# Optimization experiments

Hardware: AMD Instinct MI355X
Metric: run time of the kernel (lower is better)

## Reference

```python
import jax, jax.numpy as jnp
import numpy as np

N_NODES = 50000
N_EDGES = 800000
IN_C, HID_C, OUT_C = 256, 512, 256
DROP_P = 0.5


def _glorot(key, fan_in, fan_out):
    lim = float(np.sqrt(6.0 / (fan_in + fan_out)))
    return jax.random.uniform(key, (fan_in, fan_out), jnp.float32, -lim, lim)


def setup_inputs() -> dict:
    key = jax.random.key(0)
    k_x, k_e, k_w1, k_w2 = jax.random.split(key, 4)
    tensor = jax.random.normal(k_x, (N_NODES, IN_C), dtype=jnp.float32)
    edge_index = jax.random.randint(k_e, (2, N_EDGES), 0, N_NODES, dtype=jnp.int64)
    W1 = _glorot(k_w1, IN_C, HID_C)
    b1 = jnp.zeros((HID_C,), jnp.float32)
    W2 = _glorot(k_w2, HID_C, OUT_C)
    b2 = jnp.zeros((OUT_C,), jnp.float32)
    return {"tensor": tensor, "edge_index": edge_index,
            "W1": W1, "b1": b1, "W2": W2, "b2": b2}


def _gcn_conv(x, W, b, row, col, n_nodes):
    # PyG GCNConv: x' = D^-1/2 (A + I) D^-1/2 (x W) + b
    x = x @ W                                            # [N, F_out]
    # degree over targets including self-loops
    deg = jax.ops.segment_sum(jnp.ones_like(col, dtype=x.dtype), col,
                              num_segments=n_nodes) + 1.0
    dinv = jnp.where(deg > 0, jax.lax.rsqrt(deg), 0.0)   # [N]
    norm = dinv[row] * dinv[col]                         # [E]
    msg = x[row] * norm[:, None]                         # [E, F_out] gather
    out = jax.ops.segment_sum(msg, col, num_segments=n_nodes)  # scatter-add
    out = out + x * (dinv * dinv)[:, None]               # self-loop term
    return out + b


def _dropout(x, key, p=DROP_P):
    keep = jax.random.bernoulli(key, 1.0 - p, x.shape)
    return jnp.where(keep, x / (1.0 - p), 0.0)


def reference(tensor, edge_index, W1, b1, W2, b2):
    row, col = edge_index[0], edge_index[1]
    k1, k2 = jax.random.split(jax.random.key(42))
    x = _gcn_conv(tensor, W1, b1, row, col, N_NODES)
    x = _dropout(jax.nn.relu(x), k1)
    x = _gcn_conv(x, W2, b2, row, col, N_NODES)
    x = _dropout(jax.nn.relu(x), k2)
    return x
```

## Files before the change

### kernel.cpp

```cpp
#include <hip/hip_runtime.h>
#include <stdint.h>


#define N_NODES 50000
#define N_EDGES 800000
#define M_PAD   50048
#define IN_C 256
#define HID_C 512
#define OUT_C 256

typedef __attribute__((ext_vector_type(8))) short bf16x8;
typedef __attribute__((ext_vector_type(4))) float f32x4;

struct U2 { unsigned a, b; };

__host__ __device__ constexpr unsigned rotl32(unsigned x, int d) {
  return (x << d) | (x >> (32 - d));
}

#define TF_ROUND(r) { x0 += x1; x1 = rotl32(x1, (r)); x1 ^= x0; }

__host__ __device__ constexpr U2 threefry2x32(unsigned k0, unsigned k1,
                                              unsigned x0, unsigned x1) {
  unsigned ks2 = k0 ^ k1 ^ 0x1BD11BDAu;
  x0 += k0; x1 += k1;
  TF_ROUND(13) TF_ROUND(15) TF_ROUND(26) TF_ROUND(6)  x0 += k1;  x1 += ks2 + 1u;
  TF_ROUND(17) TF_ROUND(29) TF_ROUND(16) TF_ROUND(24) x0 += ks2; x1 += k0 + 2u;
  TF_ROUND(13) TF_ROUND(15) TF_ROUND(26) TF_ROUND(6)  x0 += k0;  x1 += k1 + 3u;
  TF_ROUND(17) TF_ROUND(29) TF_ROUND(16) TF_ROUND(24) x0 += k1;  x1 += ks2 + 4u;
  TF_ROUND(13) TF_ROUND(15) TF_ROUND(26) TF_ROUND(6)  x0 += ks2; x1 += k0 + 5u;
  return U2{x0, x1};
}

__device__ __forceinline__ ushort f2b(float f) {
  unsigned u = __builtin_bit_cast(unsigned, f);
  unsigned r = (u + 0x7fffu + ((u >> 16) & 1u)) >> 16;
  return (ushort)r;
}
__device__ __forceinline__ float b2f(ushort h) {
  unsigned u = (unsigned)h << 16;
  return __builtin_bit_cast(float, u);
}

__device__ __forceinline__ void gload16(const void* g, void* l) {
  __builtin_amdgcn_global_load_lds(
      (const __attribute__((address_space(1))) void*)g,
      (__attribute__((address_space(3))) void*)l, 16, 0, 0);
}

__global__ void deg_kernel(const int* __restrict__ col, int* __restrict__ cnt, int E) {
  int e = blockIdx.x * 256 + threadIdx.x;
  if (e < E) atomicAdd(&cnt[col[e]], 1);
}

__global__ void dinv_kernel(const int* __restrict__ cnt, float* __restrict__ dinv, int N) {
  int n = blockIdx.x * 256 + threadIdx.x;
  if (n < N) dinv[n] = rsqrtf((float)cnt[n] + 1.0f);
}

__global__ __launch_bounds__(1024) void scan_local(const int* __restrict__ cnt,
                                                   int* __restrict__ indptr,
                                                   int* __restrict__ chunkSums, int n) {
  __shared__ int s[1024];
  int gid = blockIdx.x * 1024 + threadIdx.x;
  int v = (gid < n) ? cnt[gid] : 0;
  s[threadIdx.x] = v;
  __syncthreads();
#pragma unroll
  for (int off = 1; off < 1024; off <<= 1) {
    int t = (threadIdx.x >= off) ? s[threadIdx.x - off] : 0;
    __syncthreads();
    s[threadIdx.x] += t;
    __syncthreads();
  }
  if (gid < n) indptr[gid] = s[threadIdx.x] - v;
  if (threadIdx.x == 1023) chunkSums[blockIdx.x] = s[1023];
}

__global__ void scan_chunks(int* __restrict__ chunkSums, int nChunks) {
  if (threadIdx.x == 0 && blockIdx.x == 0) {
    int acc = 0;
    for (int i = 0; i < nChunks; ++i) { int t = chunkSums[i]; chunkSums[i] = acc; acc += t; }
  }
}

__global__ void add_offsets(int* __restrict__ indptr, const int* __restrict__ chunkSums,
                            int n, int total) {
  int gid = blockIdx.x * 256 + threadIdx.x;
  if (gid < n) indptr[gid] += chunkSums[gid >> 10];
  if (gid == 0) indptr[n] = total;
}

__global__ void build_csr(const int* __restrict__ row, const int* __restrict__ col,
                          const int* __restrict__ indptr, int* __restrict__ cursor,
                          const float* __restrict__ dinv,
                          int2* __restrict__ srcW, int E) {
  int e = blockIdx.x * 256 + threadIdx.x;
  if (e < E) {
    int r = row[e];
    int c = col[e];
    int p = indptr[c] + atomicAdd(&cursor[c], 1);
    srcW[p] = make_int2(r, __builtin_bit_cast(int, dinv[r]));
  }
}

__global__ void cvt_f32_bf16(const float* __restrict__ in, ushort* __restrict__ out, int n4) {
  int i = blockIdx.x * 256 + threadIdx.x;
  if (i < n4) {
    float4 v = *(const float4*)(in + (size_t)i * 4);
    ushort4 o = make_ushort4(f2b(v.x), f2b(v.y), f2b(v.z), f2b(v.w));
    *(ushort4*)(out + (size_t)i * 4) = o;
  }
}

template <int LOGK>
__global__ void wT_kernel(const float* __restrict__ W, ushort* __restrict__ WT, int N, int total) {
  int i = blockIdx.x * 256 + threadIdx.x;
  if (i < total) {
    int k = i & ((1 << LOGK) - 1);
    int n = i >> LOGK;
    WT[i] = f2b(W[(size_t)k * N + n]);
  }
}

#define ROW_ACC(vv, ww)                                                        \
  { a0 += b2f((vv).x) * (ww); a1 += b2f((vv).y) * (ww);                        \
    a2 += b2f((vv).z) * (ww); a3 += b2f((vv).w) * (ww); }

template <bool EPI>
__global__ __launch_bounds__(256) void gather8(const ushort* __restrict__ X,
                                               const int* __restrict__ indptr,
                                               const int2* __restrict__ srcW,
                                               const float* __restrict__ dinv,
                                               const float* __restrict__ bias,
                                               void* __restrict__ outp,
                                               unsigned char* __restrict__ maskGen,
                                               const unsigned char* __restrict__ maskUse,
                                               unsigned kk0, unsigned kk1, int N) {
  int wid = (blockIdx.x * 256 + threadIdx.x) >> 6;
  int lane = threadIdx.x & 63;
  if (wid >= N) return;
  int beg = __builtin_amdgcn_readfirstlane(indptr[wid]);
  int end = __builtin_amdgcn_readfirstlane(indptr[wid + 1]);
  float dc = dinv[wid];
  const int f0 = lane * 4;
  ushort4 sv = *(const ushort4*)(X + (size_t)wid * 256 + f0);
  float a0 = b2f(sv.x) * dc, a1 = b2f(sv.y) * dc,
        a2 = b2f(sv.z) * dc, a3 = b2f(sv.w) * dc;

  int e = beg;
  for (; e + 8 <= end; e += 8) {
    int2 p0 = srcW[e + 0], p1 = srcW[e + 1], p2 = srcW[e + 2], p3 = srcW[e + 3];
    int2 p4 = srcW[e + 4], p5 = srcW[e + 5], p6 = srcW[e + 6], p7 = srcW[e + 7];
    ushort4 v0 = *(const ushort4*)(X + (size_t)p0.x * 256 + f0);
    ushort4 v1 = *(const ushort4*)(X + (size_t)p1.x * 256 + f0);
    ushort4 v2 = *(const ushort4*)(X + (size_t)p2.x * 256 + f0);
    ushort4 v3 = *(const ushort4*)(X + (size_t)p3.x * 256 + f0);
    ushort4 v4 = *(const ushort4*)(X + (size_t)p4.x * 256 + f0);
    ushort4 v5 = *(const ushort4*)(X + (size_t)p5.x * 256 + f0);
    ushort4 v6 = *(const ushort4*)(X + (size_t)p6.x * 256 + f0);
    ushort4 v7 = *(const ushort4*)(X + (size_t)p7.x * 256 + f0);
    ROW_ACC(v0, __builtin_bit_cast(float, p0.y));
    ROW_ACC(v1, __builtin_bit_cast(float, p1.y));
    ROW_ACC(v2, __builtin_bit_cast(float, p2.y));
    ROW_ACC(v3, __builtin_bit_cast(float, p3.y));
    ROW_ACC(v4, __builtin_bit_cast(float, p4.y));
    ROW_ACC(v5, __builtin_bit_cast(float, p5.y));
    ROW_ACC(v6, __builtin_bit_cast(float, p6.y));
    ROW_ACC(v7, __builtin_bit_cast(float, p7.y));
  }
  for (; e + 2 <= end; e += 2) {
    int2 p0 = srcW[e + 0], p1 = srcW[e + 1];
    ushort4 v0 = *(const ushort4*)(X + (size_t)p0.x * 256 + f0);
    ushort4 v1 = *(const ushort4*)(X + (size_t)p1.x * 256 + f0);
    ROW_ACC(v0, __builtin_bit_cast(float, p0.y));
    ROW_ACC(v1, __builtin_bit_cast(float, p1.y));
  }
  if (e < end) {
    int2 p0 = srcW[e];
    ushort4 v0 = *(const ushort4*)(X + (size_t)p0.x * 256 + f0);
    ROW_ACC(v0, __builtin_bit_cast(float, p0.y));
  }
  a0 *= dc; a1 *= dc; a2 *= dc; a3 *= dc;

  if (EPI) {
    float4 bv = *(const float4*)(bias + f0);
    unsigned mk = maskUse[(size_t)wid * 32 + (lane >> 1)];
    int sh = (lane & 1) * 4;
    float v0 = fmaxf(a0 + bv.x, 0.f);
    float v1 = fmaxf(a1 + bv.y, 0.f);
    float v2 = fmaxf(a2 + bv.z, 0.f);
    float v3 = fmaxf(a3 + bv.w, 0.f);
    v0 = ((mk >> (sh + 0)) & 1u) ? 0.f : v0 * 2.0f;
    v1 = ((mk >> (sh + 1)) & 1u) ? 0.f : v1 * 2.0f;
    v2 = ((mk >> (sh + 2)) & 1u) ? 0.f : v2 * 2.0f;
    v3 = ((mk >> (sh + 3)) & 1u) ? 0.f : v3 * 2.0f;
    *(float4*)((float*)outp + (size_t)wid * 256 + f0) = make_float4(v0, v1, v2, v3);
  } else {
    uint2 o;
    o.x = (unsigned)f2b(a0) | ((unsigned)f2b(a1) << 16);
    o.y = (unsigned)f2b(a2) | ((unsigned)f2b(a3) << 16);
    *(uint2*)((ushort*)outp + (size_t)wid * 256 + f0) = o;
    unsigned gl = (unsigned)wid * 64u + (unsigned)lane;
    unsigned eb = gl * 8u;
    unsigned byte = 0;
#pragma unroll
    for (int j = 0; j < 8; ++j) {
      U2 r = threefry2x32(kk0, kk1, 0u, eb + (unsigned)j);
      byte |= (((r.a ^ r.b) >> 31) & 1u) << j;
    }
    maskGen[gl] = (unsigned char)byte;
  }
}

template <int MODE>
__global__ __launch_bounds__(256) void gemm_bf16(const ushort* __restrict__ A,
                                                 const ushort* __restrict__ BT,
                                                 ushort* __restrict__ C,
                                                 int M, int K, int N,
                                                 const float* __restrict__ bias,
                                                 const unsigned char* __restrict__ mask1,
                                                 unsigned char* __restrict__ maskOut,
                                                 unsigned kk0, unsigned kk1) {
  __shared__ __align__(16) ushort lds[16384];
  const int tid = threadIdx.x;
  const int lane = tid & 63;
  const int wv = tid >> 6;
  const int wr = wv >> 1, wc = wv & 1;
  const int bm = blockIdx.x * 128;
  const int bn = blockIdx.y * 128;

  f32x4 acc[4][4] = {};
  const int xorv = (lane & 7) << 4;

  const int nt = K >> 6;
  for (int t = 0; t < nt; ++t) {
    const int k0 = t << 6;
#pragma unroll
    for (int l = 0; l < 4; ++l) {
      int cid = l * 256 + tid;
      int row = cid >> 3;
      int kcol = ((cid & 7) ^ (row & 7)) * 8;
      gload16(A + (size_t)(bm + row) * K + k0 + kcol, (void*)(lds + cid * 8));
      gload16(BT + (size_t)(bn + row) * K + k0 + kcol, (void*)(lds + 8192 + cid * 8));
    }
    __syncthreads();
    const char* Ab = (const char*)lds;
    const char* Bb = (const char*)(lds + 8192);
#pragma unroll
    for (int ks = 0; ks < 2; ++ks) {
      bf16x8 af[4], bf[4];
      const int kb = (ks * 64 + (lane >> 4) * 16) ^ xorv;
#pragma unroll
      for (int i = 0; i < 4; ++i) {
        int arow = wr * 64 + i * 16 + (lane & 15);
        af[i] = *(const bf16x8*)(Ab + arow * 128 + kb);
        int brow = wc * 64 + i * 16 + (lane & 15);
        bf[i] = *(const bf16x8*)(Bb + brow * 128 + kb);
      }
#pragma unroll
      for (int m = 0; m < 4; ++m)
#pragma unroll
        for (int n = 0; n < 4; ++n)
          acc[m][n] = __builtin_amdgcn_mfma_f32_16x16x32_bf16(bf[n], af[m], acc[m][n], 0, 0, 0);
    }
    __syncthreads();
  }

  const int growb = bm + wr * 64 + (lane & 15);
  const int gcolb = bn + wc * 64 + ((lane >> 4) << 2);
  float4 bias_v[4];
  if (MODE == 1) {
#pragma unroll
    for (int n = 0; n < 4; ++n) bias_v[n] = *(const float4*)(bias + gcolb + n * 16);
  }
#pragma unroll
  for (int m = 0; m < 4; ++m) {
    int grow = growb + m * 16;
    unsigned long long mrow = 0;
    if (MODE == 1)
      mrow = *(const unsigned long long*)(mask1 + (((size_t)grow * N + bn + wc * 64) >> 3));
#pragma unroll
    for (int n = 0; n < 4; ++n) {
      int gcol = gcolb + n * 16;
      float v[4];
#pragma unroll
      for (int r = 0; r < 4; ++r) {
        float x = acc[m][n][r];
        if (MODE == 1) {
          x = fmaxf(x + ((const float*)&bias_v[n])[r], 0.f);
          int bit = (gcol - (bn + wc * 64)) + r;
          x = ((mrow >> bit) & 1ull) ? 0.f : x * 2.0f;
        }
        v[r] = x;
      }
      uint2 o;
      o.x = (unsigned)f2b(v[0]) | ((unsigned)f2b(v[1]) << 16);
      o.y = (unsigned)f2b(v[2]) | ((unsigned)f2b(v[3]) << 16);
      *(uint2*)(C + (size_t)grow * N + gcol) = o;
    }
  }

  if (MODE == 2) {
    int row = tid >> 1, ch = (tid & 1) * 64;
    int grow = bm + row;
    unsigned base = (unsigned)grow * (unsigned)N + (unsigned)(bn + ch);
    unsigned long long mword = 0;
#pragma unroll
    for (int j = 0; j < 64; ++j) {
      U2 rr = threefry2x32(kk0, kk1, 0u, base + (unsigned)j);
      mword |= (unsigned long long)(((rr.a ^ rr.b) >> 31) & 1u) << j;
    }
    *(unsigned long long*)(maskOut + (size_t)(base >> 3)) = mword;
  }
}

extern "C" void kernel_launch(void* const* d_in, const int* in_sizes, int n_in,
                              void* d_out, int out_size, void* d_ws, size_t ws_size,
                              hipStream_t stream) {
  const float* x  = (const float*)d_in[0];
  const int*   ei = (const int*)d_in[1];
  const float* W1 = (const float*)d_in[2];
  const float* b1 = (const float*)d_in[3];
  const float* W2 = (const float*)d_in[4];
  const float* b2 = (const float*)d_in[5];
  float* out = (float*)d_out;
  (void)in_sizes; (void)n_in; (void)out_size; (void)ws_size;

  const int* row = ei;
  const int* col = ei + N_EDGES;

  char* ws = (char*)d_ws;
  float*  dinv      = (float*) (ws);
  int*    cnt       = (int*)   (ws + (1u << 18));
  int*    indptr    = (int*)   (ws + (2u << 18));
  int*    cursor    = (int*)   (ws + (3u << 18));
  int*    chunkSums = (int*)   (ws + (1u << 20));
  int2*   srcW      = (int2*)  (ws + 2u * (1u << 20));
  ushort* W1T       = (ushort*)(ws + 9u * (1u << 20));
  ushort* W2T       = (ushort*)(ws + 9u * (1u << 20) + (1u << 19));
  unsigned char* mask1 = (unsigned char*)(ws + 10u * (1u << 20));
  unsigned char* mask2 = (unsigned char*)(ws + 14u * (1u << 20));
  ushort* x16       = (ushort*)(ws + 18u * (1u << 20));
  ushort* aggB      = (ushort*)(ws + 44u * (1u << 20));
  ushort* h         = (ushort*)(ws + 70u * (1u << 20));
  ushort* hw2       = (ushort*)(ws + 122u* (1u << 20));

  constexpr U2 K1 = threefry2x32(0u, 42u, 0u, 0u);
  constexpr U2 K2 = threefry2x32(0u, 42u, 0u, 1u);

  (void)hipMemsetAsync(cnt, 0, N_NODES * sizeof(int), stream);
  (void)hipMemsetAsync(cursor, 0, N_NODES * sizeof(int), stream);
  deg_kernel<<<(N_EDGES + 255) / 256, 256, 0, stream>>>(col, cnt, N_EDGES);
  dinv_kernel<<<(N_NODES + 255) / 256, 256, 0, stream>>>(cnt, dinv, N_NODES);
  const int nChunks = (N_NODES + 1023) / 1024;
  scan_local<<<nChunks, 1024, 0, stream>>>(cnt, indptr, chunkSums, N_NODES);
  scan_chunks<<<1, 64, 0, stream>>>(chunkSums, nChunks);
  add_offsets<<<(N_NODES + 255) / 256, 256, 0, stream>>>(indptr, chunkSums, N_NODES, N_EDGES);
  build_csr<<<(N_EDGES + 255) / 256, 256, 0, stream>>>(row, col, indptr, cursor, dinv, srcW, N_EDGES);

  cvt_f32_bf16<<<(N_NODES * IN_C / 4 + 255) / 256, 256, 0, stream>>>(x, x16, N_NODES * IN_C / 4);
  wT_kernel<8><<<(IN_C * HID_C + 255) / 256, 256, 0, stream>>>(W1, W1T, HID_C, IN_C * HID_C);
  wT_kernel<9><<<(HID_C * OUT_C + 255) / 256, 256, 0, stream>>>(W2, W2T, OUT_C, HID_C * OUT_C);
  (void)hipMemsetAsync(aggB + (size_t)N_NODES * IN_C, 0, (size_t)(M_PAD - N_NODES) * IN_C * 2, stream);

  gather8<false><<<(N_NODES + 3) / 4, 256, 0, stream>>>(
      x16, indptr, srcW, dinv, nullptr, aggB, mask1, nullptr, K1.a, K1.b, N_NODES);
  gemm_bf16<1><<<dim3(M_PAD / 128, HID_C / 128), 256, 0, stream>>>(
      aggB, W1T, h, M_PAD, IN_C, HID_C, b1, mask1, nullptr, 0u, 0u);

  gemm_bf16<2><<<dim3(M_PAD / 128, OUT_C / 128), 256, 0, stream>>>(
      h, W2T, hw2, M_PAD, HID_C, OUT_C, nullptr, nullptr, mask2, K2.a, K2.b);
  gather8<true><<<(N_NODES + 3) / 4, 256, 0, stream>>>(
      hw2, indptr, srcW, dinv, b2, out, nullptr, mask2, 0u, 0u, N_NODES);
}
```

Measured before the change: 350.0 us.

## Move dropout-2 mask generation into first gather and remap GEMM blocks per XCD

Layer-2 dropout mask generation (threefry) moves out of the second GEMM epilogue and into the first, memory-bound gather kernel, where the hash arithmetic can hide behind gather latency. The dinv computation is folded into scan_local, and the two weight-transpose kernels are merged into one, removing several small launches. The GEMMs switch to a 1D grid with an XCD-aware block remap, so adjacent N-tiles of the same M rows land on the same XCD for L2 reuse of A. The cost is that the first gather does extra hash work in half its lanes and the GEMM tile indexing becomes more complex.

```diff
diff --git a/kernel.cpp b/kernel.cpp
--- a/kernel.cpp
+++ b/kernel.cpp
@@ -53,17 +53,14 @@
   if (e < E) atomicAdd(&cnt[col[e]], 1);
 }
 
-__global__ void dinv_kernel(const int* __restrict__ cnt, float* __restrict__ dinv, int N) {
-  int n = blockIdx.x * 256 + threadIdx.x;
-  if (n < N) dinv[n] = rsqrtf((float)cnt[n] + 1.0f);
-}
-
 __global__ __launch_bounds__(1024) void scan_local(const int* __restrict__ cnt,
                                                    int* __restrict__ indptr,
-                                                   int* __restrict__ chunkSums, int n) {
+                                                   int* __restrict__ chunkSums,
+                                                   float* __restrict__ dinv, int n) {
   __shared__ int s[1024];
   int gid = blockIdx.x * 1024 + threadIdx.x;
   int v = (gid < n) ? cnt[gid] : 0;
+  if (gid < n) dinv[gid] = rsqrtf((float)v + 1.0f);
   s[threadIdx.x] = v;
   __syncthreads();
 #pragma unroll
@@ -113,13 +110,18 @@
   }
 }
 
-template <int LOGK>
-__global__ void wT_kernel(const float* __restrict__ W, ushort* __restrict__ WT, int N, int total) {
+__global__ void wT_both(const float* __restrict__ W1, const float* __restrict__ W2,
+                        ushort* __restrict__ W1T, ushort* __restrict__ W2T) {
   int i = blockIdx.x * 256 + threadIdx.x;
-  if (i < total) {
-    int k = i & ((1 << LOGK) - 1);
-    int n = i >> LOGK;
-    WT[i] = f2b(W[(size_t)k * N + n]);
+  if (i < IN_C * HID_C) {
+    int k = i & (IN_C - 1);
+    int n = i >> 8;
+    W1T[i] = f2b(W1[(size_t)k * HID_C + n]);
+  } else {
+    int j = i - IN_C * HID_C;
+    int k = j & (HID_C - 1);
+    int n = j >> 9;
+    W2T[j] = f2b(W2[(size_t)k * OUT_C + n]);
   }
 }
 
@@ -134,9 +136,11 @@
                                                const float* __restrict__ dinv,
                                                const float* __restrict__ bias,
                                                void* __restrict__ outp,
-                                               unsigned char* __restrict__ maskGen,
+                                               unsigned char* __restrict__ mask1Gen,
+                                               unsigned char* __restrict__ mask2Gen,
                                                const unsigned char* __restrict__ maskUse,
-                                               unsigned kk0, unsigned kk1, int N) {
+                                               unsigned k10, unsigned k11,
+                                               unsigned k20, unsigned k21, int N) {
   int wid = (blockIdx.x * 256 + threadIdx.x) >> 6;
   int lane = threadIdx.x & 63;
   if (wid >= N) return;
@@ -201,34 +205,53 @@
     o.x = (unsigned)f2b(a0) | ((unsigned)f2b(a1) << 16);
     o.y = (unsigned)f2b(a2) | ((unsigned)f2b(a3) << 16);
     *(uint2*)((ushort*)outp + (size_t)wid * 256 + f0) = o;
-    unsigned gl = (unsigned)wid * 64u + (unsigned)lane;
-    unsigned eb = gl * 8u;
-    unsigned byte = 0;
-#pragma unroll
-    for (int j = 0; j < 8; ++j) {
-      U2 r = threefry2x32(kk0, kk1, 0u, eb + (unsigned)j);
-      byte |= (((r.a ^ r.b) >> 31) & 1u) << j;
-    }
-    maskGen[gl] = (unsigned char)byte;
-  }
-}
-
-template <int MODE>
+    {
+      unsigned gl = (unsigned)wid * 64u + (unsigned)lane;
+      unsigned eb = gl * 8u;
+      unsigned byte = 0;
+#pragma unroll
+      for (int j = 0; j < 8; ++j) {
+        U2 r = threefry2x32(k10, k11, 0u, eb + (unsigned)j);
+        byte |= (((r.a ^ r.b) >> 31) & 1u) << j;
+      }
+      mask1Gen[gl] = (unsigned char)byte;
+    }
+    if (lane < 32) {
+      unsigned eb = (unsigned)wid * 256u + (unsigned)lane * 8u;
+      unsigned byte = 0;
+#pragma unroll
+      for (int j = 0; j < 8; ++j) {
+        U2 r = threefry2x32(k20, k21, 0u, eb + (unsigned)j);
+        byte |= (((r.a ^ r.b) >> 31) & 1u) << j;
+      }
+      mask2Gen[(size_t)wid * 32 + lane] = (unsigned char)byte;
+    }
+  }
+}
+
+template <bool EPI, int NSTRIP>
 __global__ __launch_bounds__(256) void gemm_bf16(const ushort* __restrict__ A,
                                                  const ushort* __restrict__ BT,
                                                  ushort* __restrict__ C,
                                                  int M, int K, int N,
                                                  const float* __restrict__ bias,
-                                                 const unsigned char* __restrict__ mask1,
-                                                 unsigned char* __restrict__ maskOut,
-                                                 unsigned kk0, unsigned kk1) {
+                                                 const unsigned char* __restrict__ mask1) {
   __shared__ __align__(16) ushort lds[16384];
+  const int nwg = gridDim.x;
+  {
+  }
+  const int orig = blockIdx.x;
+  const int q = nwg >> 3, r = nwg & 7;
+  const int xcd = orig & 7, loc = orig >> 3;
+  const int wg = (xcd < r) ? (xcd * (q + 1) + loc)
+                           : (r * (q + 1) + (xcd - r) * q + loc);
+  const int bm = (wg / NSTRIP) * 128;
+  const int bn = (wg % NSTRIP) * 128;
+
   const int tid = threadIdx.x;
   const int lane = tid & 63;
   const int wv = tid >> 6;
   const int wr = wv >> 1, wc = wv & 1;
-  const int bm = blockIdx.x * 128;
-  const int bn = blockIdx.y * 128;
 
   f32x4 acc[4][4] = {};
   const int xorv = (lane & 7) << 4;
@@ -270,7 +293,7 @@
   const int growb = bm + wr * 64 + (lane & 15);
   const int gcolb = bn + wc * 64 + ((lane >> 4) << 2);
   float4 bias_v[4];
-  if (MODE == 1) {
+  if (EPI) {
 #pragma unroll
     for (int n = 0; n < 4; ++n) bias_v[n] = *(const float4*)(bias + gcolb + n * 16);
   }
@@ -278,40 +301,27 @@
   for (int m = 0; m < 4; ++m) {
     int grow = growb + m * 16;
     unsigned long long mrow = 0;
-    if (MODE == 1)
+    if (EPI)
       mrow = *(const unsigned long long*)(mask1 + (((size_t)grow * N + bn + wc * 64) >> 3));
 #pragma unroll
     for (int n = 0; n < 4; ++n) {
       int gcol = gcolb + n * 16;
       float v[4];
 #pragma unroll
-      for (int r = 0; r < 4; ++r) {
-        float x = acc[m][n][r];
-        if (MODE == 1) {
-          x = fmaxf(x + ((const float*)&bias_v[n])[r], 0.f);
-          int bit = (gcol - (bn + wc * 64)) + r;
+      for (int r2 = 0; r2 < 4; ++r2) {
+        float x = acc[m][n][r2];
+        if (EPI) {
+          x = fmaxf(x + ((const float*)&bias_v[n])[r2], 0.f);
+          int bit = (gcol - (bn + wc * 64)) + r2;
           x = ((mrow >> bit) & 1ull) ? 0.f : x * 2.0f;
         }
-        v[r] = x;
+        v[r2] = x;
       }
       uint2 o;
       o.x = (unsigned)f2b(v[0]) | ((unsigned)f2b(v[1]) << 16);
       o.y = (unsigned)f2b(v[2]) | ((unsigned)f2b(v[3]) << 16);
       *(uint2*)(C + (size_t)grow * N + gcol) = o;
     }
-  }
-
-  if (MODE == 2) {
-    int row = tid >> 1, ch = (tid & 1) * 64;
-    int grow = bm + row;
-    unsigned base = (unsigned)grow * (unsigned)N + (unsigned)(bn + ch);
-    unsigned long long mword = 0;
-#pragma unroll
-    for (int j = 0; j < 64; ++j) {
-      U2 rr = threefry2x32(kk0, kk1, 0u, base + (unsigned)j);
-      mword |= (unsigned long long)(((rr.a ^ rr.b) >> 31) & 1u) << j;
-    }
-    *(unsigned long long*)(maskOut + (size_t)(base >> 3)) = mword;
   }
 }
 
@@ -352,25 +362,25 @@
   (void)hipMemsetAsync(cnt, 0, N_NODES * sizeof(int), stream);
   (void)hipMemsetAsync(cursor, 0, N_NODES * sizeof(int), stream);
   deg_kernel<<<(N_EDGES + 255) / 256, 256, 0, stream>>>(col, cnt, N_EDGES);
-  dinv_kernel<<<(N_NODES + 255) / 256, 256, 0, stream>>>(cnt, dinv, N_NODES);
   const int nChunks = (N_NODES + 1023) / 1024;
-  scan_local<<<nChunks, 1024, 0, stream>>>(cnt, indptr, chunkSums, N_NODES);
+  scan_local<<<nChunks, 1024, 0, stream>>>(cnt, indptr, chunkSums, dinv, N_NODES);
   scan_chunks<<<1, 64, 0, stream>>>(chunkSums, nChunks);
   add_offsets<<<(N_NODES + 255) / 256, 256, 0, stream>>>(indptr, chunkSums, N_NODES, N_EDGES);
   build_csr<<<(N_EDGES + 255) / 256, 256, 0, stream>>>(row, col, indptr, cursor, dinv, srcW, N_EDGES);
 
   cvt_f32_bf16<<<(N_NODES * IN_C / 4 + 255) / 256, 256, 0, stream>>>(x, x16, N_NODES * IN_C / 4);
-  wT_kernel<8><<<(IN_C * HID_C + 255) / 256, 256, 0, stream>>>(W1, W1T, HID_C, IN_C * HID_C);
-  wT_kernel<9><<<(HID_C * OUT_C + 255) / 256, 256, 0, stream>>>(W2, W2T, OUT_C, HID_C * OUT_C);
+  wT_both<<<(IN_C * HID_C + HID_C * OUT_C + 255) / 256, 256, 0, stream>>>(W1, W2, W1T, W2T);
   (void)hipMemsetAsync(aggB + (size_t)N_NODES * IN_C, 0, (size_t)(M_PAD - N_NODES) * IN_C * 2, stream);
 
   gather8<false><<<(N_NODES + 3) / 4, 256, 0, stream>>>(
-      x16, indptr, srcW, dinv, nullptr, aggB, mask1, nullptr, K1.a, K1.b, N_NODES);
-  gemm_bf16<1><<<dim3(M_PAD / 128, HID_C / 128), 256, 0, stream>>>(
-      aggB, W1T, h, M_PAD, IN_C, HID_C, b1, mask1, nullptr, 0u, 0u);
-
-  gemm_bf16<2><<<dim3(M_PAD / 128, OUT_C / 128), 256, 0, stream>>>(
-      h, W2T, hw2, M_PAD, HID_C, OUT_C, nullptr, nullptr, mask2, K2.a, K2.b);
+      x16, indptr, srcW, dinv, nullptr, aggB, mask1, mask2, nullptr,
+      K1.a, K1.b, K2.a, K2.b, N_NODES);
+  gemm_bf16<true, HID_C / 128><<<(M_PAD / 128) * (HID_C / 128), 256, 0, stream>>>(
+      aggB, W1T, h, M_PAD, IN_C, HID_C, b1, mask1);
+
+  gemm_bf16<false, OUT_C / 128><<<(M_PAD / 128) * (OUT_C / 128), 256, 0, stream>>>(
+      h, W2T, hw2, M_PAD, HID_C, OUT_C, nullptr, nullptr);
   gather8<true><<<(N_NODES + 3) / 4, 256, 0, stream>>>(
-      hw2, indptr, srcW, dinv, b2, out, nullptr, mask2, 0u, 0u, N_NODES);
-}
+      hw2, indptr, srcW, dinv, b2, out, nullptr, nullptr, mask2,
+      0u, 0u, 0u, 0u, N_NODES);
+}
```

New measurement: 359.2 us. +2.6%, slower.
